# Optimization experiments

Hardware: AMD Instinct MI355X
Metric: run time of the kernel (lower is better)

## Reference

```python
import jax, jax.numpy as jnp
import numpy as np

N_NODES = 500_000
N_EDGES = 16_000_000
F_IN = 4
C = 4


def setup_inputs() -> dict:
    key = jax.random.key(0)
    ks = jax.random.split(key, 8)
    x = jax.random.normal(ks[0], (N_NODES, F_IN), dtype=jnp.float32)
    edge_index = jax.random.randint(ks[1], (2, N_EDGES), 0, N_NODES, dtype=jnp.int32)
    node = 1000  # node id whose incident edges are scored
    # GCNConv weights (PyG lin weight is [out,in]; math is x @ W with W=[in,out]) + separate bias
    W1 = jax.random.normal(ks[2], (F_IN, C), dtype=jnp.float32) * 0.5
    b1 = jnp.zeros((C,), dtype=jnp.float32)
    W2 = jax.random.normal(ks[3], (C, C), dtype=jnp.float32) * 0.5
    b2 = jnp.zeros((C,), dtype=jnp.float32)
    Wr = jax.random.normal(ks[4], (C, 1), dtype=jnp.float32) * 0.5
    br = jnp.zeros((1,), dtype=jnp.float32)
    return {"x": x, "edge_index": edge_index, "node": node,
            "W1": W1, "b1": b1, "W2": W2, "b2": b2, "Wr": Wr, "br": br}


def reference(x, edge_index, node, W1, b1, W2, b2, Wr, br):
    n = x.shape[0]
    src, dst = edge_index[0], edge_index[1]
    # GCN normalization with added self-loops (PyG gcn_norm, edge_weight=1)
    loop = jnp.arange(n, dtype=src.dtype)
    srcl = jnp.concatenate([src, loop])  # [E+N]
    dstl = jnp.concatenate([dst, loop])
    deg = jax.ops.segment_sum(jnp.ones(srcl.shape[0], dtype=x.dtype), dstl, num_segments=n)
    dinv = jnp.where(deg > 0, jax.lax.rsqrt(deg), jnp.zeros_like(deg))
    norm = (dinv[srcl] * dinv[dstl])[:, None]  # [E+N, 1]

    def gcn_conv(h, W, b):
        hW = h @ W                                  # tiny GEMM [N,C]
        msg = hW[srcl] * norm                       # edge gather + normalize [E+N, C]
        return jax.ops.segment_sum(msg, dstl, num_segments=n) + b  # scatter-add

    h = jax.nn.relu(gcn_conv(x, W1, b1))
    h = jax.nn.relu(gcn_conv(h, W2, b2))

    # Edges incident to `node`; softmax restricted to them (others masked out)
    mask = (src == node) | (dst == node)            # [E]
    targets = jnp.where(src == node, dst, src)      # other endpoint (node itself for self-loop)
    logits = (h[targets] @ Wr + br)[:, 0]           # [E]
    neg = jnp.finfo(logits.dtype).min
    score = jax.nn.softmax(jnp.where(mask, logits, neg))  # masked entries -> 0
    targets_out = jnp.where(mask, targets, -1)
    return score, targets_out
```

## Files before the change

### kernel.cpp

```cpp
#include <hip/hip_runtime.h>

#define CAP_I   65536
#define CAP_S1  (1 << 18)
#define CAP_L2  (1 << 20)
#define CAP_L1  (1 << 22)
#define LBUF_B  512
#define LBUF_C  1024
#define CBT_W   977
#define CBS_W   1954

typedef unsigned int uint;
typedef float vfloat4 __attribute__((ext_vector_type(4)));

__global__ void k_passA(const int4* __restrict__ src4, const int4* __restrict__ dst4, int nvec,
                        const int* __restrict__ nodep,
                        int* __restrict__ cnts, int* __restrict__ le, int* __restrict__ lt,
                        uint* __restrict__ bmT, uint* __restrict__ bmS1,
                        uint* __restrict__ bmS0,
                        uint* __restrict__ cbmT, uint* __restrict__ cbmS1,
                        int* __restrict__ s1list,
                        int* __restrict__ deg, float4* __restrict__ acc1,
                        float4* __restrict__ acc2) {
    const float4 z4 = make_float4(0.f, 0.f, 0.f, 0.f);
    int node = *nodep;
    int stride = gridDim.x * blockDim.x;
    for (int v = blockIdx.x * blockDim.x + threadIdx.x; v < nvec; v += stride) {
        int4 s4 = src4[v];
        int4 d4 = dst4[v];
        int ss[4] = {s4.x, s4.y, s4.z, s4.w};
        int dd[4] = {d4.x, d4.y, d4.z, d4.w};
#pragma unroll
        for (int k = 0; k < 4; k++) {
            if (ss[k] == node || dd[k] == node) {
                int t = (ss[k] == node) ? dd[k] : ss[k];
                int pos = atomicAdd(&cnts[0], 1);
                if (pos < CAP_I) { le[pos] = v * 4 + k; lt[pos] = t; }
                uint bit = 1u << (t & 31);
                atomicOr(&bmT[t >> 5], bit);
                atomicOr(&cbmT[t >> 9], 1u << ((t >> 4) & 31));
                uint old = atomicOr(&bmS1[t >> 5], bit);
                if (!(old & bit)) {
                    atomicOr(&bmS0[t >> 5], bit);
                    atomicOr(&cbmS1[t >> 8], 1u << ((t >> 3) & 31));
                    deg[t] = 0; acc1[t] = z4; acc2[t] = z4;
                    int p = atomicAdd(&cnts[2], 1);
                    if (p < CAP_S1) s1list[p] = t;
                }
            }
        }
    }
}

__global__ __launch_bounds__(256) void k_passB(
        const int* __restrict__ src, const int4* __restrict__ dst4, int nvec,
        const uint* __restrict__ cbmT, const uint* __restrict__ bmT,
        uint* __restrict__ bmS1, uint* __restrict__ bmS0, uint* __restrict__ cbmS1,
        int* __restrict__ cnts, int* __restrict__ l2s, int* __restrict__ l2t,
        int* __restrict__ s1list,
        int* __restrict__ deg, float4* __restrict__ acc1, float4* __restrict__ acc2) {
    __shared__ uint lcb[CBT_W];
    __shared__ int bes[LBUF_B], bet[LBUF_B], bs1[LBUF_B];
    __shared__ int lcE, lcS, gbE, gbS;
    for (int i = threadIdx.x; i < CBT_W; i += blockDim.x) lcb[i] = cbmT[i];
    if (threadIdx.x == 0) { lcE = 0; lcS = 0; }
    __syncthreads();
    const float4 z4 = make_float4(0.f, 0.f, 0.f, 0.f);
    int stride = gridDim.x * blockDim.x;
    for (int v = blockIdx.x * blockDim.x + threadIdx.x; v < nvec; v += stride) {
        int4 d4 = dst4[v];
        int dd[4] = {d4.x, d4.y, d4.z, d4.w};
#pragma unroll
        for (int k = 0; k < 4; k++) {
            int d = dd[k];
            if ((lcb[d >> 9] >> ((d >> 4) & 31)) & 1u) {
                if ((bmT[d >> 5] >> (d & 31)) & 1u) {
                    int s = src[v * 4 + k];
                    int p = atomicAdd(&lcE, 1);
                    if (p < LBUF_B) { bes[p] = s; bet[p] = d; }
                    else { int g = atomicAdd(&cnts[1], 1);
                           if (g < CAP_L2) { l2s[g] = s; l2t[g] = d; } }
                    uint bit = 1u << (s & 31);
                    uint old = atomicOr(&bmS1[s >> 5], bit);
                    if (!(old & bit)) {
                        atomicOr(&bmS0[s >> 5], bit);
                        atomicOr(&cbmS1[s >> 8], 1u << ((s >> 3) & 31));
                        deg[s] = 0; acc1[s] = z4; acc2[s] = z4;
                        int q = atomicAdd(&lcS, 1);
                        if (q < LBUF_B) bs1[q] = s;
                        else { int g = atomicAdd(&cnts[2], 1);
                               if (g < CAP_S1) s1list[g] = s; }
                    }
                }
            }
        }
    }
    __syncthreads();
    int nE = min(lcE, LBUF_B), nS = min(lcS, LBUF_B);
    if (threadIdx.x == 0) {
        gbE = (nE > 0) ? atomicAdd(&cnts[1], nE) : 0;
        gbS = (nS > 0) ? atomicAdd(&cnts[2], nS) : 0;
    }
    __syncthreads();
    for (int i = threadIdx.x; i < nE; i += blockDim.x) {
        int pos = gbE + i;
        if (pos < CAP_L2) { l2s[pos] = bes[i]; l2t[pos] = bet[i]; }
    }
    for (int i = threadIdx.x; i < nS; i += blockDim.x) {
        int pos = gbS + i;
        if (pos < CAP_S1) s1list[pos] = bs1[i];
    }
}

__global__ __launch_bounds__(256) void k_passC(
        const int* __restrict__ src, const int4* __restrict__ dst4, int nvec,
        const uint* __restrict__ cbmS1, const uint* __restrict__ bmS1,
        uint* __restrict__ bmS0,
        int* __restrict__ cnts, int* __restrict__ l1s, int* __restrict__ l1t,
        int* __restrict__ deg) {
    __shared__ uint lcb[CBS_W];
    __shared__ int lbs[LBUF_C], lbt[LBUF_C];
    __shared__ int lcnt, gbase;
    for (int i = threadIdx.x; i < CBS_W; i += blockDim.x) lcb[i] = cbmS1[i];
    if (threadIdx.x == 0) lcnt = 0;
    __syncthreads();
    int stride = gridDim.x * blockDim.x;
    for (int v = blockIdx.x * blockDim.x + threadIdx.x; v < nvec; v += stride) {
        int4 d4 = dst4[v];
        int dd[4] = {d4.x, d4.y, d4.z, d4.w};
#pragma unroll
        for (int k = 0; k < 4; k++) {
            int d = dd[k];
            if ((lcb[d >> 8] >> ((d >> 3) & 31)) & 1u) {
                if ((bmS1[d >> 5] >> (d & 31)) & 1u) {
                    int s = src[v * 4 + k];
                    uint bit = 1u << (s & 31);
                    uint old = atomicOr(&bmS0[s >> 5], bit);
                    if (!(old & bit)) deg[s] = 0;
                    int p = atomicAdd(&lcnt, 1);
                    if (p < LBUF_C) { lbs[p] = s; lbt[p] = d; }
                    else { int g = atomicAdd(&cnts[3], 1);
                           if (g < CAP_L1) { l1s[g] = s; l1t[g] = d; } }
                }
            }
        }
    }
    __syncthreads();
    int n = min(lcnt, LBUF_C);
    if (threadIdx.x == 0) gbase = (n > 0) ? atomicAdd(&cnts[3], n) : 0;
    __syncthreads();
    for (int i = threadIdx.x; i < n; i += blockDim.x) {
        int pos = gbase + i;
        if (pos < CAP_L1) { l1s[pos] = lbs[i]; l1t[pos] = lbt[i]; }
    }
}

__global__ __launch_bounds__(256) void k_passD(
        const int4* __restrict__ dst4, int nvec,
        const uint* __restrict__ bmS0, int* __restrict__ deg,
        vfloat4* __restrict__ out_score4, vfloat4* __restrict__ out_tgt4) {
    const vfloat4 zero = {0.f, 0.f, 0.f, 0.f};
    const vfloat4 neg1 = {-1.f, -1.f, -1.f, -1.f};
    int stride = gridDim.x * blockDim.x;
    for (int v = blockIdx.x * blockDim.x + threadIdx.x; v < nvec; v += stride) {
        int4 d4 = dst4[v];
        __builtin_nontemporal_store(zero, &out_score4[v]);
        __builtin_nontemporal_store(neg1, &out_tgt4[v]);
        int dd[4] = {d4.x, d4.y, d4.z, d4.w};
#pragma unroll
        for (int k = 0; k < 4; k++) {
            int d = dd[k];
            if ((bmS0[d >> 5] >> (d & 31)) & 1u) atomicAdd(&deg[d], 1);
        }
    }
}

__global__ void k_conv1(const int* __restrict__ cnts, const int* __restrict__ l1s,
                        const int* __restrict__ l1t, const float* __restrict__ x,
                        const float* __restrict__ W1, const int* __restrict__ deg,
                        float* __restrict__ acc1) {
    int n = cnts[3]; if (n > CAP_L1) n = CAP_L1;
    int stride = gridDim.x * blockDim.x;
    for (int j = blockIdx.x * blockDim.x + threadIdx.x; j < n; j += stride) {
        int s = l1s[j], d = l1t[j];
        float4 xv = *(const float4*)(x + (size_t)s * 4);
        float dis = rsqrtf((float)deg[s] + 1.0f);
        float o0 = (xv.x * W1[0] + xv.y * W1[4] + xv.z * W1[8]  + xv.w * W1[12]) * dis;
        float o1 = (xv.x * W1[1] + xv.y * W1[5] + xv.z * W1[9]  + xv.w * W1[13]) * dis;
        float o2 = (xv.x * W1[2] + xv.y * W1[6] + xv.z * W1[10] + xv.w * W1[14]) * dis;
        float o3 = (xv.x * W1[3] + xv.y * W1[7] + xv.z * W1[11] + xv.w * W1[15]) * dis;
        float* a = acc1 + (size_t)d * 4;
        atomicAdd(a + 0, o0); atomicAdd(a + 1, o1);
        atomicAdd(a + 2, o2); atomicAdd(a + 3, o3);
    }
}

__global__ __launch_bounds__(1024) void k_tail(
        const int* __restrict__ cnts, const int* __restrict__ s1list,
        const int* __restrict__ l2s, const int* __restrict__ l2t,
        const int* __restrict__ le, const int* __restrict__ lt,
        const float* __restrict__ x, const float* __restrict__ W1,
        const float* __restrict__ b1, const float* __restrict__ W2,
        const float* __restrict__ b2, const float* __restrict__ Wr,
        const float* __restrict__ br, const int* __restrict__ deg,
        const float* __restrict__ acc1, float* __restrict__ acc2,
        float* __restrict__ gB, float* __restrict__ z,
        float* __restrict__ out_score, float* __restrict__ out_tgt) {
    int tid = threadIdx.x;
    int n2 = cnts[2]; if (n2 > CAP_S1) n2 = CAP_S1;
    for (int j = tid; j < n2; j += blockDim.x) {
        int i = s1list[j];
        float di = rsqrtf((float)deg[i] + 1.0f);
        float4 xv = *(const float4*)(x + (size_t)i * 4);
        float4 a  = *(const float4*)(acc1 + (size_t)i * 4);
        float w0 = xv.x * W1[0] + xv.y * W1[4] + xv.z * W1[8]  + xv.w * W1[12];
        float w1 = xv.x * W1[1] + xv.y * W1[5] + xv.z * W1[9]  + xv.w * W1[13];
        float w2 = xv.x * W1[2] + xv.y * W1[6] + xv.z * W1[10] + xv.w * W1[14];
        float w3 = xv.x * W1[3] + xv.y * W1[7] + xv.z * W1[11] + xv.w * W1[15];
        float h0 = fmaxf((a.x + w0 * di) * di + b1[0], 0.f);
        float h1 = fmaxf((a.y + w1 * di) * di + b1[1], 0.f);
        float h2 = fmaxf((a.z + w2 * di) * di + b1[2], 0.f);
        float h3 = fmaxf((a.w + w3 * di) * di + b1[3], 0.f);
        float4 o;
        o.x = (h0 * W2[0] + h1 * W2[4] + h2 * W2[8]  + h3 * W2[12]) * di;
        o.y = (h0 * W2[1] + h1 * W2[5] + h2 * W2[9]  + h3 * W2[13]) * di;
        o.z = (h0 * W2[2] + h1 * W2[6] + h2 * W2[10] + h3 * W2[14]) * di;
        o.w = (h0 * W2[3] + h1 * W2[7] + h2 * W2[11] + h3 * W2[15]) * di;
        *(float4*)(gB + (size_t)i * 4) = o;
    }
    __syncthreads();
    int nL2 = cnts[1]; if (nL2 > CAP_L2) nL2 = CAP_L2;
    for (int j = tid; j < nL2; j += blockDim.x) {
        int s = l2s[j], t = l2t[j];
        float4 g = *(const float4*)(gB + (size_t)s * 4);
        float* a = acc2 + (size_t)t * 4;
        atomicAdd(a + 0, g.x); atomicAdd(a + 1, g.y);
        atomicAdd(a + 2, g.z); atomicAdd(a + 3, g.w);
    }
    __syncthreads();
    int nI = cnts[0]; if (nI > CAP_I) nI = CAP_I;
    for (int j = tid; j < nI; j += blockDim.x) {
        int t = lt[j];
        float di = rsqrtf((float)deg[t] + 1.0f);
        float4 a = *(const float4*)(acc2 + (size_t)t * 4);
        float4 g = *(const float4*)(gB + (size_t)t * 4);
        float h0 = fmaxf((a.x + g.x) * di + b2[0], 0.f);
        float h1 = fmaxf((a.y + g.y) * di + b2[1], 0.f);
        float h2 = fmaxf((a.z + g.z) * di + b2[2], 0.f);
        float h3 = fmaxf((a.w + g.w) * di + b2[3], 0.f);
        z[t] = h0 * Wr[0] + h1 * Wr[1] + h2 * Wr[2] + h3 * Wr[3] + br[0];
    }
    __syncthreads();
    if (tid == 0) {
        float m = -3.402823466e+38f;
        for (int k = 0; k < nI; k++) m = fmaxf(m, z[lt[k]]);
        float ssum = 0.f;
        for (int k = 0; k < nI; k++) ssum += __expf(z[lt[k]] - m);
        float inv = (ssum > 0.f) ? 1.f / ssum : 0.f;
        for (int k = 0; k < nI; k++) {
            out_score[le[k]] = __expf(z[lt[k]] - m) * inv;
            out_tgt[le[k]]   = (float)lt[k];
        }
    }
}

extern "C" void kernel_launch(void* const* d_in, const int* in_sizes, int n_in,
                              void* d_out, int out_size, void* d_ws, size_t ws_size,
                              hipStream_t stream) {
    const float* x  = (const float*)d_in[0];
    const int*   ei = (const int*)d_in[1];
    const int*   nodep = (const int*)d_in[2];
    const float* W1 = (const float*)d_in[3];
    const float* b1 = (const float*)d_in[4];
    const float* W2 = (const float*)d_in[5];
    const float* b2 = (const float*)d_in[6];
    const float* Wr = (const float*)d_in[7];
    const float* br = (const float*)d_in[8];

    const int N = in_sizes[0] / 4;
    const int E = in_sizes[1] / 2;
    const int nvec = E / 4;
    const int NW = (N + 31) / 32;
    const int* src = ei;
    const int* dst = ei + E;

    char* ws = (char*)d_ws;
    size_t off = 0;
    auto alloc = [&](size_t bytes) { char* p = ws + off; off = (off + bytes + 255) & ~(size_t)255; return p; };
    char* zero_base = ws;
    uint*  bmT    = (uint*) alloc((size_t)NW * 4);
    uint*  bmS1   = (uint*) alloc((size_t)NW * 4);
    uint*  bmS0   = (uint*) alloc((size_t)NW * 4);
    uint*  cbmT   = (uint*) alloc((size_t)CBT_W * 4);
    uint*  cbmS1  = (uint*) alloc((size_t)CBS_W * 4);
    int*   cnts   = (int*)  alloc(256);
    size_t zero_len = off;
    int*   deg    = (int*)  alloc((size_t)N * 4);
    float* acc1   = (float*)alloc((size_t)N * 16);
    float* acc2   = (float*)alloc((size_t)N * 16);
    float* gB     = (float*)alloc((size_t)N * 16);
    float* z      = (float*)alloc((size_t)N * 4);
    int*   le     = (int*)  alloc((size_t)CAP_I * 4);
    int*   lt     = (int*)  alloc((size_t)CAP_I * 4);
    int*   s1list = (int*)  alloc((size_t)CAP_S1 * 4);
    int*   l2s    = (int*)  alloc((size_t)CAP_L2 * 4);
    int*   l2t    = (int*)  alloc((size_t)CAP_L2 * 4);
    int*   l1s    = (int*)  alloc((size_t)CAP_L1 * 4);
    int*   l1t    = (int*)  alloc((size_t)CAP_L1 * 4);

    float* out_score = (float*)d_out;
    float* out_tgt   = out_score + E;

    int edgeBlocksA = (nvec + 255) / 256;
    if (edgeBlocksA > 2048) edgeBlocksA = 2048;

    (void)hipMemsetAsync(zero_base, 0, zero_len, stream);

    k_passA<<<edgeBlocksA, 256, 0, stream>>>((const int4*)src, (const int4*)dst, nvec, nodep,
                                             cnts, le, lt, bmT, bmS1, bmS0, cbmT, cbmS1,
                                             s1list, deg, (float4*)acc1, (float4*)acc2);
    k_passB<<<2048, 256, 0, stream>>>(src, (const int4*)dst, nvec, cbmT, bmT,
                                      bmS1, bmS0, cbmS1, cnts, l2s, l2t, s1list,
                                      deg, (float4*)acc1, (float4*)acc2);
    k_passC<<<2048, 256, 0, stream>>>(src, (const int4*)dst, nvec, cbmS1, bmS1, bmS0,
                                      cnts, l1s, l1t, deg);
    k_passD<<<4096, 256, 0, stream>>>((const int4*)dst, nvec, bmS0, deg,
                                      (vfloat4*)out_score, (vfloat4*)out_tgt);
    k_conv1<<<256, 256, 0, stream>>>(cnts, l1s, l1t, x, W1, deg, acc1);
    k_tail<<<1, 1024, 0, stream>>>(cnts, s1list, l2s, l2t, le, lt, x, W1, b1, W2, b2,
                                   Wr, br, deg, acc1, acc2, gB, z, out_score, out_tgt);
}
```

Before: 281.3 us.

## Split degree counters into eight memset-zeroed replicas to spread atomic contention

Degree counting now goes to eight replicated int arrays, one per block-index residue. The readers sum the eight copies when they need a degree. The replicas live inside the memset-zeroed region, so the per-node deg=0 resets and the test-and-set atomic in passC can go. The change also raises the block count of passes A, B and C to 4096. In exchange the memset grows by 16 MB, and every degree lookup in conv1 and the tail does eight scattered loads.

```diff
diff --git a/kernel.cpp b/kernel.cpp
--- a/kernel.cpp
+++ b/kernel.cpp
@@ -12,6 +12,13 @@
 typedef unsigned int uint;
 typedef float vfloat4 __attribute__((ext_vector_type(4)));
 
+__device__ __forceinline__ float deg_sum(const int* __restrict__ d8, int N, int i) {
+    int s = 0;
+#pragma unroll
+    for (int j = 0; j < 8; j++) s += d8[(size_t)j * N + i];
+    return (float)s;
+}
+
 __global__ void k_passA(const int4* __restrict__ src4, const int4* __restrict__ dst4, int nvec,
                         const int* __restrict__ nodep,
                         int* __restrict__ cnts, int* __restrict__ le, int* __restrict__ lt,
@@ -19,8 +26,7 @@
                         uint* __restrict__ bmS0,
                         uint* __restrict__ cbmT, uint* __restrict__ cbmS1,
                         int* __restrict__ s1list,
-                        int* __restrict__ deg, float4* __restrict__ acc1,
-                        float4* __restrict__ acc2) {
+                        float4* __restrict__ acc1, float4* __restrict__ acc2) {
     const float4 z4 = make_float4(0.f, 0.f, 0.f, 0.f);
     int node = *nodep;
     int stride = gridDim.x * blockDim.x;
@@ -33,17 +39,17 @@
         for (int k = 0; k < 4; k++) {
             if (ss[k] == node || dd[k] == node) {
                 int t = (ss[k] == node) ? dd[k] : ss[k];
-                int pos = atomicAdd(&cnts[0], 1);
+                int pos = atomicAdd(cnts + 0, 1);
                 if (pos < CAP_I) { le[pos] = v * 4 + k; lt[pos] = t; }
                 uint bit = 1u << (t & 31);
-                atomicOr(&bmT[t >> 5], bit);
-                atomicOr(&cbmT[t >> 9], 1u << ((t >> 4) & 31));
-                uint old = atomicOr(&bmS1[t >> 5], bit);
+                atomicOr(bmT + (t >> 5), bit);
+                atomicOr(cbmT + (t >> 9), 1u << ((t >> 4) & 31));
+                uint old = atomicOr(bmS1 + (t >> 5), bit);
                 if (!(old & bit)) {
-                    atomicOr(&bmS0[t >> 5], bit);
-                    atomicOr(&cbmS1[t >> 8], 1u << ((t >> 3) & 31));
-                    deg[t] = 0; acc1[t] = z4; acc2[t] = z4;
-                    int p = atomicAdd(&cnts[2], 1);
+                    atomicOr(bmS0 + (t >> 5), bit);
+                    atomicOr(cbmS1 + (t >> 8), 1u << ((t >> 3) & 31));
+                    acc1[t] = z4; acc2[t] = z4;
+                    int p = atomicAdd(cnts + 2, 1);
                     if (p < CAP_S1) s1list[p] = t;
                 }
             }
@@ -57,7 +63,7 @@
         uint* __restrict__ bmS1, uint* __restrict__ bmS0, uint* __restrict__ cbmS1,
         int* __restrict__ cnts, int* __restrict__ l2s, int* __restrict__ l2t,
         int* __restrict__ s1list,
-        int* __restrict__ deg, float4* __restrict__ acc1, float4* __restrict__ acc2) {
+        float4* __restrict__ acc1, float4* __restrict__ acc2) {
     __shared__ uint lcb[CBT_W];
     __shared__ int bes[LBUF_B], bet[LBUF_B], bs1[LBUF_B];
     __shared__ int lcE, lcS, gbE, gbS;
@@ -77,17 +83,17 @@
                     int s = src[v * 4 + k];
                     int p = atomicAdd(&lcE, 1);
                     if (p < LBUF_B) { bes[p] = s; bet[p] = d; }
-                    else { int g = atomicAdd(&cnts[1], 1);
+                    else { int g = atomicAdd(cnts + 1, 1);
                            if (g < CAP_L2) { l2s[g] = s; l2t[g] = d; } }
                     uint bit = 1u << (s & 31);
-                    uint old = atomicOr(&bmS1[s >> 5], bit);
+                    uint old = atomicOr(bmS1 + (s >> 5), bit);
                     if (!(old & bit)) {
-                        atomicOr(&bmS0[s >> 5], bit);
-                        atomicOr(&cbmS1[s >> 8], 1u << ((s >> 3) & 31));
-                        deg[s] = 0; acc1[s] = z4; acc2[s] = z4;
+                        atomicOr(bmS0 + (s >> 5), bit);
+                        atomicOr(cbmS1 + (s >> 8), 1u << ((s >> 3) & 31));
+                        acc1[s] = z4; acc2[s] = z4;
                         int q = atomicAdd(&lcS, 1);
                         if (q < LBUF_B) bs1[q] = s;
-                        else { int g = atomicAdd(&cnts[2], 1);
+                        else { int g = atomicAdd(cnts + 2, 1);
                                if (g < CAP_S1) s1list[g] = s; }
                     }
                 }
@@ -97,8 +103,8 @@
     __syncthreads();
     int nE = min(lcE, LBUF_B), nS = min(lcS, LBUF_B);
     if (threadIdx.x == 0) {
-        gbE = (nE > 0) ? atomicAdd(&cnts[1], nE) : 0;
-        gbS = (nS > 0) ? atomicAdd(&cnts[2], nS) : 0;
+        gbE = (nE > 0) ? atomicAdd(cnts + 1, nE) : 0;
+        gbS = (nS > 0) ? atomicAdd(cnts + 2, nS) : 0;
     }
     __syncthreads();
     for (int i = threadIdx.x; i < nE; i += blockDim.x) {
@@ -115,8 +121,7 @@
         const int* __restrict__ src, const int4* __restrict__ dst4, int nvec,
         const uint* __restrict__ cbmS1, const uint* __restrict__ bmS1,
         uint* __restrict__ bmS0,
-        int* __restrict__ cnts, int* __restrict__ l1s, int* __restrict__ l1t,
-        int* __restrict__ deg) {
+        int* __restrict__ cnts, int* __restrict__ l1s, int* __restrict__ l1t) {
     __shared__ uint lcb[CBS_W];
     __shared__ int lbs[LBUF_C], lbt[LBUF_C];
     __shared__ int lcnt, gbase;
@@ -133,12 +138,10 @@
             if ((lcb[d >> 8] >> ((d >> 3) & 31)) & 1u) {
                 if ((bmS1[d >> 5] >> (d & 31)) & 1u) {
                     int s = src[v * 4 + k];
-                    uint bit = 1u << (s & 31);
-                    uint old = atomicOr(&bmS0[s >> 5], bit);
-                    if (!(old & bit)) deg[s] = 0;
+                    atomicOr(bmS0 + (s >> 5), 1u << (s & 31));
                     int p = atomicAdd(&lcnt, 1);
                     if (p < LBUF_C) { lbs[p] = s; lbt[p] = d; }
-                    else { int g = atomicAdd(&cnts[3], 1);
+                    else { int g = atomicAdd(cnts + 3, 1);
                            if (g < CAP_L1) { l1s[g] = s; l1t[g] = d; } }
                 }
             }
@@ -146,7 +149,7 @@
     }
     __syncthreads();
     int n = min(lcnt, LBUF_C);
-    if (threadIdx.x == 0) gbase = (n > 0) ? atomicAdd(&cnts[3], n) : 0;
+    if (threadIdx.x == 0) gbase = (n > 0) ? atomicAdd(cnts + 3, n) : 0;
     __syncthreads();
     for (int i = threadIdx.x; i < n; i += blockDim.x) {
         int pos = gbase + i;
@@ -155,35 +158,36 @@
 }
 
 __global__ __launch_bounds__(256) void k_passD(
-        const int4* __restrict__ dst4, int nvec,
-        const uint* __restrict__ bmS0, int* __restrict__ deg,
+        const int4* __restrict__ dst4, int nvec, int N,
+        const uint* __restrict__ bmS0, int* __restrict__ d8,
         vfloat4* __restrict__ out_score4, vfloat4* __restrict__ out_tgt4) {
     const vfloat4 zero = {0.f, 0.f, 0.f, 0.f};
     const vfloat4 neg1 = {-1.f, -1.f, -1.f, -1.f};
+    int* dloc = d8 + (size_t)(blockIdx.x & 7) * N;
     int stride = gridDim.x * blockDim.x;
     for (int v = blockIdx.x * blockDim.x + threadIdx.x; v < nvec; v += stride) {
         int4 d4 = dst4[v];
-        __builtin_nontemporal_store(zero, &out_score4[v]);
-        __builtin_nontemporal_store(neg1, &out_tgt4[v]);
+        __builtin_nontemporal_store(zero, out_score4 + v);
+        __builtin_nontemporal_store(neg1, out_tgt4 + v);
         int dd[4] = {d4.x, d4.y, d4.z, d4.w};
 #pragma unroll
         for (int k = 0; k < 4; k++) {
             int d = dd[k];
-            if ((bmS0[d >> 5] >> (d & 31)) & 1u) atomicAdd(&deg[d], 1);
+            if ((bmS0[d >> 5] >> (d & 31)) & 1u) atomicAdd(dloc + d, 1);
         }
     }
 }
 
 __global__ void k_conv1(const int* __restrict__ cnts, const int* __restrict__ l1s,
                         const int* __restrict__ l1t, const float* __restrict__ x,
-                        const float* __restrict__ W1, const int* __restrict__ deg,
+                        const float* __restrict__ W1, const int* __restrict__ d8, int N,
                         float* __restrict__ acc1) {
     int n = cnts[3]; if (n > CAP_L1) n = CAP_L1;
     int stride = gridDim.x * blockDim.x;
     for (int j = blockIdx.x * blockDim.x + threadIdx.x; j < n; j += stride) {
         int s = l1s[j], d = l1t[j];
         float4 xv = *(const float4*)(x + (size_t)s * 4);
-        float dis = rsqrtf((float)deg[s] + 1.0f);
+        float dis = rsqrtf(deg_sum(d8, N, s) + 1.0f);
         float o0 = (xv.x * W1[0] + xv.y * W1[4] + xv.z * W1[8]  + xv.w * W1[12]) * dis;
         float o1 = (xv.x * W1[1] + xv.y * W1[5] + xv.z * W1[9]  + xv.w * W1[13]) * dis;
         float o2 = (xv.x * W1[2] + xv.y * W1[6] + xv.z * W1[10] + xv.w * W1[14]) * dis;
@@ -201,7 +205,7 @@
         const float* __restrict__ x, const float* __restrict__ W1,
         const float* __restrict__ b1, const float* __restrict__ W2,
         const float* __restrict__ b2, const float* __restrict__ Wr,
-        const float* __restrict__ br, const int* __restrict__ deg,
+        const float* __restrict__ br, const int* __restrict__ d8, int N,
         const float* __restrict__ acc1, float* __restrict__ acc2,
         float* __restrict__ gB, float* __restrict__ z,
         float* __restrict__ out_score, float* __restrict__ out_tgt) {
@@ -209,7 +213,7 @@
     int n2 = cnts[2]; if (n2 > CAP_S1) n2 = CAP_S1;
     for (int j = tid; j < n2; j += blockDim.x) {
         int i = s1list[j];
-        float di = rsqrtf((float)deg[i] + 1.0f);
+        float di = rsqrtf(deg_sum(d8, N, i) + 1.0f);
         float4 xv = *(const float4*)(x + (size_t)i * 4);
         float4 a  = *(const float4*)(acc1 + (size_t)i * 4);
         float w0 = xv.x * W1[0] + xv.y * W1[4] + xv.z * W1[8]  + xv.w * W1[12];
@@ -240,7 +244,7 @@
     int nI = cnts[0]; if (nI > CAP_I) nI = CAP_I;
     for (int j = tid; j < nI; j += blockDim.x) {
         int t = lt[j];
-        float di = rsqrtf((float)deg[t] + 1.0f);
+        float di = rsqrtf(deg_sum(d8, N, t) + 1.0f);
         float4 a = *(const float4*)(acc2 + (size_t)t * 4);
         float4 g = *(const float4*)(gB + (size_t)t * 4);
         float h0 = fmaxf((a.x + g.x) * di + b2[0], 0.f);
@@ -293,8 +297,8 @@
     uint*  cbmT   = (uint*) alloc((size_t)CBT_W * 4);
     uint*  cbmS1  = (uint*) alloc((size_t)CBS_W * 4);
     int*   cnts   = (int*)  alloc(256);
+    int*   d8     = (int*)  alloc((size_t)8 * N * 4);
     size_t zero_len = off;
-    int*   deg    = (int*)  alloc((size_t)N * 4);
     float* acc1   = (float*)alloc((size_t)N * 16);
     float* acc2   = (float*)alloc((size_t)N * 16);
     float* gB     = (float*)alloc((size_t)N * 16);
@@ -310,22 +314,22 @@
     float* out_score = (float*)d_out;
     float* out_tgt   = out_score + E;
 
-    int edgeBlocksA = (nvec + 255) / 256;
-    if (edgeBlocksA > 2048) edgeBlocksA = 2048;
+    int edgeBlocks = (nvec + 255) / 256;
+    if (edgeBlocks > 4096) edgeBlocks = 4096;
 
     (void)hipMemsetAsync(zero_base, 0, zero_len, stream);
 
-    k_passA<<<edgeBlocksA, 256, 0, stream>>>((const int4*)src, (const int4*)dst, nvec, nodep,
-                                             cnts, le, lt, bmT, bmS1, bmS0, cbmT, cbmS1,
-                                             s1list, deg, (float4*)acc1, (float4*)acc2);
-    k_passB<<<2048, 256, 0, stream>>>(src, (const int4*)dst, nvec, cbmT, bmT,
-                                      bmS1, bmS0, cbmS1, cnts, l2s, l2t, s1list,
-                                      deg, (float4*)acc1, (float4*)acc2);
-    k_passC<<<2048, 256, 0, stream>>>(src, (const int4*)dst, nvec, cbmS1, bmS1, bmS0,
-                                      cnts, l1s, l1t, deg);
-    k_passD<<<4096, 256, 0, stream>>>((const int4*)dst, nvec, bmS0, deg,
+    k_passA<<<edgeBlocks, 256, 0, stream>>>((const int4*)src, (const int4*)dst, nvec, nodep,
+                                            cnts, le, lt, bmT, bmS1, bmS0, cbmT, cbmS1,
+                                            s1list, (float4*)acc1, (float4*)acc2);
+    k_passB<<<edgeBlocks, 256, 0, stream>>>(src, (const int4*)dst, nvec, cbmT, bmT,
+                                            bmS1, bmS0, cbmS1, cnts, l2s, l2t, s1list,
+                                            (float4*)acc1, (float4*)acc2);
+    k_passC<<<edgeBlocks, 256, 0, stream>>>(src, (const int4*)dst, nvec, cbmS1, bmS1, bmS0,
+                                            cnts, l1s, l1t);
+    k_passD<<<4096, 256, 0, stream>>>((const int4*)dst, nvec, N, bmS0, d8,
                                       (vfloat4*)out_score, (vfloat4*)out_tgt);
-    k_conv1<<<256, 256, 0, stream>>>(cnts, l1s, l1t, x, W1, deg, acc1);
+    k_conv1<<<256, 256, 0, stream>>>(cnts, l1s, l1t, x, W1, d8, N, acc1);
     k_tail<<<1, 1024, 0, stream>>>(cnts, s1list, l2s, l2t, le, lt, x, W1, b1, W2, b2,
-                                   Wr, br, deg, acc1, acc2, gB, z, out_score, out_tgt);
-}
+                                   Wr, br, d8, N, acc1, acc2, gB, z, out_score, out_tgt);
+}
```

Result: slower. 336.6 us (+19.7%).
